# Kernel tuning notes

Measured on AMD Instinct MI355X. Metric: run time of the kernel, lower is better.

## Reference

```python
import math
import jax, jax.numpy as jnp
import numpy as np

NUM_HEADS = 16
HEAD_DIM = 64


def circular_rel_bias(L, slope=1.0):
    idx = jnp.arange(L)
    d = jnp.abs(idx[None, :] - idx[:, None])
    d = jnp.minimum(d, L - d).astype(jnp.float32)
    return -slope * d  # [L, L]


def setup_inputs() -> dict:
    key = jax.random.key(0)
    kq, kk, kv, km = jax.random.split(key, 4)
    B, L, HD = 2, 2048, NUM_HEADS * HEAD_DIM
    return {
        "query_states": jax.random.normal(kq, (B, L, HD), dtype=jnp.float32),
        "key_states": jax.random.normal(kk, (B, L, HD), dtype=jnp.float32),
        "value_states": jax.random.normal(kv, (B, L, HD), dtype=jnp.float32),
        "mask": jax.random.randint(km, (B, L), 0, 2, dtype=jnp.int32),
    }


def reference(query_states, key_states, value_states, mask):
    B, L, _ = query_states.shape
    H, D = NUM_HEADS, HEAD_DIM
    q = query_states.reshape(B, L, H, D).transpose(0, 2, 1, 3)  # [B,H,L,D]
    k = key_states.reshape(B, L, H, D).transpose(0, 2, 1, 3)
    v = value_states.reshape(B, L, H, D).transpose(0, 2, 1, 3)

    scores = jnp.einsum("bhqd,bhkd->bhqk", q, k) / math.sqrt(D)
    scores = scores + circular_rel_bias(L)[None, None, :, :]
    # mask == 0 -> -1e9 on key positions
    scores = jnp.where((mask == 0)[:, None, None, :], jnp.float32(-1e9), scores)
    weights = jax.nn.softmax(scores, axis=-1)
    out = jnp.einsum("bhqk,bhkd->bhqd", weights, v)
    return out.transpose(0, 2, 1, 3).reshape(B, L, H * D)
```

## Files before the change

kernel.cpp:

```cpp
#include <hip/hip_runtime.h>

#define NH 16
#define HD 64
#define LSEQ 2048
#define BQ 128
#define BK 64
#define NQT (LSEQ / BQ)
#define RS (NH * HD)
#define NTILE 4

typedef __bf16 bf16x8 __attribute__((ext_vector_type(8)));
typedef float f32x4 __attribute__((ext_vector_type(4)));

#define EXP_NEG8 0.00033546262790251185f

__global__ __launch_bounds__(512, 4)
void attn_kernel(const float* __restrict__ Q,
                 const float* __restrict__ K,
                 const float* __restrict__ V,
                 const int* __restrict__ Mk,
                 float* __restrict__ Out)
{
    __shared__ alignas(16) char smem_raw[4 * 64 * 72 * 2];
    __shared__ alignas(16) __bf16 sP[8][16][72];
    __bf16* kvb = (__bf16*)smem_raw;

    const int tid  = threadIdx.x;
    const int wave = tid >> 6;
    const int lane = tid & 63;
    const int ln   = lane & 15;
    const int quad = lane >> 4;

    const unsigned bid = blockIdx.x;
    const unsigned w   = (bid & 7u) * 64u + (bid >> 3);
    const int qt = w & (NQT - 1);
    const int bh = w >> 4;
    const int b  = bh >> 4;
    const int h  = bh & 15;

    const int q0   = qt * BQ;
    const int qrow = q0 + wave * 16;

    const size_t bh_off = ((size_t)b * LSEQ) * RS + (size_t)h * HD;
    const float* gQ = Q + bh_off;
    const float* gK = K + bh_off;
    const float* gV = V + bh_off;
    const int*   gM = Mk + (size_t)b * LSEQ;
    float*       gO = Out + bh_off;

    int srow[2], sc4[2];
#pragma unroll
    for (int i = 0; i < 2; ++i) { int idx = tid + i * 512; srow[i] = idx >> 4; sc4[i] = idx & 15; }

    bf16x8 qfrag[2];
#pragma unroll
    for (int c = 0; c < 2; ++c) {
        const float* src = gQ + (size_t)(qrow + ln) * RS + c * 32 + quad * 8;
        float4 f0 = *(const float4*)(src);
        float4 f1 = *(const float4*)(src + 4);
        bf16x8 t;
        t[0] = (__bf16)(f0.x * 0.125f); t[1] = (__bf16)(f0.y * 0.125f);
        t[2] = (__bf16)(f0.z * 0.125f); t[3] = (__bf16)(f0.w * 0.125f);
        t[4] = (__bf16)(f1.x * 0.125f); t[5] = (__bf16)(f1.y * 0.125f);
        t[6] = (__bf16)(f1.z * 0.125f); t[7] = (__bf16)(f1.w * 0.125f);
        qfrag[c] = t;
    }

    f32x4 o_acc[4];
#pragma unroll
    for (int i = 0; i < 4; ++i) o_acc[i] = f32x4{0.f, 0.f, 0.f, 0.f};
    float l_part[4] = {0.f, 0.f, 0.f, 0.f};

    int k0s[NTILE];
#pragma unroll
    for (int j = 0; j < NTILE; ++j) k0s[j] = ((2 * qt + 31 + j) & 31) * BK;

    float4 kreg[2], vreg[2];
    int mr[4];
#pragma unroll
    for (int i = 0; i < 2; ++i) {
        kreg[i] = *(const float4*)(gK + (size_t)(k0s[0] + srow[i]) * RS + sc4[i] * 4);
        vreg[i] = *(const float4*)(gV + (size_t)(k0s[0] + srow[i]) * RS + sc4[i] * 4);
    }
#pragma unroll
    for (int t = 0; t < 4; ++t) mr[t] = gM[k0s[0] + t * 16 + ln];

#pragma unroll
    for (int j = 0; j < NTILE; ++j) {
        const int bb = j & 1;
        __bf16* sKb = kvb + bb * 4608;
        __bf16* sVb = kvb + 9216 + bb * 4608;

#pragma unroll
        for (int i = 0; i < 2; ++i) {
            float4 f = kreg[i];
            __bf16* dst = sKb + srow[i] * 72 + sc4[i] * 4;
            dst[0] = (__bf16)f.x; dst[1] = (__bf16)f.y;
            dst[2] = (__bf16)f.z; dst[3] = (__bf16)f.w;
            float4 g = vreg[i];
            const int vk = srow[i] ^ ((sc4[i] & 7) << 3);
            sVb[(sc4[i] * 4 + 0) * 72 + vk] = (__bf16)g.x;
            sVb[(sc4[i] * 4 + 1) * 72 + vk] = (__bf16)g.y;
            sVb[(sc4[i] * 4 + 2) * 72 + vk] = (__bf16)g.z;
            sVb[(sc4[i] * 4 + 3) * 72 + vk] = (__bf16)g.w;
        }
        float mm[4];
#pragma unroll
        for (int t = 0; t < 4; ++t) mm[t] = mr[t] ? EXP_NEG8 : 0.f;

        if (j + 1 < NTILE) {
            const int k0n = k0s[j + 1];
#pragma unroll
            for (int i = 0; i < 2; ++i) {
                kreg[i] = *(const float4*)(gK + (size_t)(k0n + srow[i]) * RS + sc4[i] * 4);
                vreg[i] = *(const float4*)(gV + (size_t)(k0n + srow[i]) * RS + sc4[i] * 4);
            }
#pragma unroll
            for (int t = 0; t < 4; ++t) mr[t] = gM[k0n + t * 16 + ln];
        }
        __syncthreads();

        const int k0 = k0s[j];
        f32x4 s[4];
#pragma unroll
        for (int t = 0; t < 4; ++t) {
            f32x4 acc = f32x4{0.f, 0.f, 0.f, 0.f};
#pragma unroll
            for (int ch = 0; ch < 2; ++ch) {
                bf16x8 bk = *(const bf16x8*)(sKb + (t * 16 + ln) * 72 + ch * 32 + quad * 8);
                acc = __builtin_amdgcn_mfma_f32_16x16x32_bf16(qfrag[ch], bk, acc, 0, 0, 0);
            }
            s[t] = acc;
        }

        const int qg0 = qrow + quad * 4;
#pragma unroll
        for (int t = 0; t < 4; ++t) {
            const int kg = k0 + t * 16 + ln;
#pragma unroll
            for (int r = 0; r < 4; ++r) {
                int dd = qg0 + r - kg; dd = dd < 0 ? -dd : dd;
                int d2 = LSEQ - dd; dd = d2 < dd ? d2 : dd;
                float p = __expf(s[t][r] - (float)dd) * mm[t];
                l_part[r] += p;
                sP[wave][quad * 4 + r][(t * 16 + ln) ^ (quad << 3)] = (__bf16)p;
            }
        }

#pragma unroll
        for (int ch = 0; ch < 2; ++ch) {
            bf16x8 pa = *(const bf16x8*)&sP[wave][ln][(ch * 32 + quad * 8) ^ ((ln >> 2) << 3)];
#pragma unroll
            for (int nt = 0; nt < 4; ++nt) {
                const int vr = nt * 16 + ln;
                const int vc = (ch * 32 + quad * 8) ^ (((vr >> 2) & 7) << 3);
                bf16x8 bv = *(const bf16x8*)(sVb + vr * 72 + vc);
                o_acc[nt] = __builtin_amdgcn_mfma_f32_16x16x32_bf16(pa, bv, o_acc[nt], 0, 0, 0);
            }
        }
    }

    float inv[4];
#pragma unroll
    for (int r = 0; r < 4; ++r) {
        float l = l_part[r];
#pragma unroll
        for (int off = 1; off < 16; off <<= 1)
            l += __shfl_xor(l, off, 64);
        inv[r] = 1.f / l;
    }

    __syncthreads();
    float* oscr = (float*)smem_raw;
#pragma unroll
    for (int r = 0; r < 4; ++r)
#pragma unroll
        for (int nt = 0; nt < 4; ++nt)
            oscr[(wave * 16 + quad * 4 + r) * 68 + nt * 16 + ln] = o_acc[nt][r] * inv[r];
    __syncthreads();

#pragma unroll
    for (int p = 0; p < 4; ++p) {
        int f   = tid + p * 512;
        int row = f >> 4;
        int c4  = f & 15;
        float4 val = *(const float4*)&oscr[row * 68 + c4 * 4];
        *(float4*)(gO + (size_t)(q0 + row) * RS + c4 * 4) = val;
    }
}

extern "C" void kernel_launch(void* const* d_in, const int* in_sizes, int n_in,
                              void* d_out, int out_size, void* d_ws, size_t ws_size,
                              hipStream_t stream) {
    const float* Q  = (const float*)d_in[0];
    const float* K  = (const float*)d_in[1];
    const float* V  = (const float*)d_in[2];
    const int*   Mk = (const int*)d_in[3];
    float*       O  = (float*)d_out;

    dim3 grid(2 * NH * NQT);
    dim3 block(512);
    attn_kernel<<<grid, block, 0, stream>>>(Q, K, V, Mk, O);
}
```

Before: 107.7 us.

## Keep P in registers via transposed S MFMA and permuted V layout

Computes S transposed by swapping the MFMA operands, so each lane's accumulator elements form the P operand of the PV MFMA directly. This removes the per-wave sP shared-memory round trip and the associated LDS writes and reads. V is stored with a permuted key slot so the register P ordering matches. The key mask is loaded once per tile with a ballot into a 64-bit mask, the row-sum reduction becomes fewer shuffles, and the block-index swizzle is dropped, which may change L2 locality.

```diff
diff --git a/kernel.cpp b/kernel.cpp
--- a/kernel.cpp
+++ b/kernel.cpp
@@ -22,7 +22,6 @@
                  float* __restrict__ Out)
 {
     __shared__ alignas(16) char smem_raw[4 * 64 * 72 * 2];
-    __shared__ alignas(16) __bf16 sP[8][16][72];
     __bf16* kvb = (__bf16*)smem_raw;
 
     const int tid  = threadIdx.x;
@@ -31,10 +30,8 @@
     const int ln   = lane & 15;
     const int quad = lane >> 4;
 
-    const unsigned bid = blockIdx.x;
-    const unsigned w   = (bid & 7u) * 64u + (bid >> 3);
-    const int qt = w & (NQT - 1);
-    const int bh = w >> 4;
+    const int qt = blockIdx.x & (NQT - 1);
+    const int bh = blockIdx.x >> 4;
     const int b  = bh >> 4;
     const int h  = bh & 15;
 
@@ -51,6 +48,13 @@
     int srow[2], sc4[2];
 #pragma unroll
     for (int i = 0; i < 2; ++i) { int idx = tid + i * 512; srow[i] = idx >> 4; sc4[i] = idx & 15; }
+
+    int vslot[2];
+#pragma unroll
+    for (int i = 0; i < 2; ++i) {
+        int k = srow[i];
+        vslot[i] = (k & 32) | ((k & 12) << 1) | ((k & 16) >> 2) | (k & 3);
+    }
 
     bf16x8 qfrag[2];
 #pragma unroll
@@ -69,21 +73,19 @@
     f32x4 o_acc[4];
 #pragma unroll
     for (int i = 0; i < 4; ++i) o_acc[i] = f32x4{0.f, 0.f, 0.f, 0.f};
-    float l_part[4] = {0.f, 0.f, 0.f, 0.f};
+    float l_part = 0.f;
 
     int k0s[NTILE];
 #pragma unroll
     for (int j = 0; j < NTILE; ++j) k0s[j] = ((2 * qt + 31 + j) & 31) * BK;
 
     float4 kreg[2], vreg[2];
-    int mr[4];
 #pragma unroll
     for (int i = 0; i < 2; ++i) {
         kreg[i] = *(const float4*)(gK + (size_t)(k0s[0] + srow[i]) * RS + sc4[i] * 4);
         vreg[i] = *(const float4*)(gV + (size_t)(k0s[0] + srow[i]) * RS + sc4[i] * 4);
     }
-#pragma unroll
-    for (int t = 0; t < 4; ++t) mr[t] = gM[k0s[0] + t * 16 + ln];
+    unsigned long long mbits = __ballot(gM[k0s[0] + lane] != 0);
 
 #pragma unroll
     for (int j = 0; j < NTILE; ++j) {
@@ -98,15 +100,13 @@
             dst[0] = (__bf16)f.x; dst[1] = (__bf16)f.y;
             dst[2] = (__bf16)f.z; dst[3] = (__bf16)f.w;
             float4 g = vreg[i];
-            const int vk = srow[i] ^ ((sc4[i] & 7) << 3);
+            const int vk = vslot[i] ^ ((sc4[i] & 7) << 3);
             sVb[(sc4[i] * 4 + 0) * 72 + vk] = (__bf16)g.x;
             sVb[(sc4[i] * 4 + 1) * 72 + vk] = (__bf16)g.y;
             sVb[(sc4[i] * 4 + 2) * 72 + vk] = (__bf16)g.z;
             sVb[(sc4[i] * 4 + 3) * 72 + vk] = (__bf16)g.w;
         }
-        float mm[4];
-#pragma unroll
-        for (int t = 0; t < 4; ++t) mm[t] = mr[t] ? EXP_NEG8 : 0.f;
+        const unsigned long long mb = mbits;
 
         if (j + 1 < NTILE) {
             const int k0n = k0s[j + 1];
@@ -115,8 +115,7 @@
                 kreg[i] = *(const float4*)(gK + (size_t)(k0n + srow[i]) * RS + sc4[i] * 4);
                 vreg[i] = *(const float4*)(gV + (size_t)(k0n + srow[i]) * RS + sc4[i] * 4);
             }
-#pragma unroll
-            for (int t = 0; t < 4; ++t) mr[t] = gM[k0n + t * 16 + ln];
+            mbits = __ballot(gM[k0n + lane] != 0);
         }
         __syncthreads();
 
@@ -127,29 +126,34 @@
             f32x4 acc = f32x4{0.f, 0.f, 0.f, 0.f};
 #pragma unroll
             for (int ch = 0; ch < 2; ++ch) {
-                bf16x8 bk = *(const bf16x8*)(sKb + (t * 16 + ln) * 72 + ch * 32 + quad * 8);
-                acc = __builtin_amdgcn_mfma_f32_16x16x32_bf16(qfrag[ch], bk, acc, 0, 0, 0);
+                bf16x8 ak = *(const bf16x8*)(sKb + (t * 16 + ln) * 72 + ch * 32 + quad * 8);
+                acc = __builtin_amdgcn_mfma_f32_16x16x32_bf16(ak, qfrag[ch], acc, 0, 0, 0);
             }
             s[t] = acc;
         }
 
-        const int qg0 = qrow + quad * 4;
+        const int qg = qrow + ln;
 #pragma unroll
         for (int t = 0; t < 4; ++t) {
-            const int kg = k0 + t * 16 + ln;
+            const unsigned nib = (unsigned)(mb >> (t * 16 + quad * 4)) & 0xFu;
 #pragma unroll
             for (int r = 0; r < 4; ++r) {
-                int dd = qg0 + r - kg; dd = dd < 0 ? -dd : dd;
+                const int kg = k0 + t * 16 + quad * 4 + r;
+                int dd = qg - kg; dd = dd < 0 ? -dd : dd;
                 int d2 = LSEQ - dd; dd = d2 < dd ? d2 : dd;
-                float p = __expf(s[t][r] - (float)dd) * mm[t];
-                l_part[r] += p;
-                sP[wave][quad * 4 + r][(t * 16 + ln) ^ (quad << 3)] = (__bf16)p;
+                float mmv = ((nib >> r) & 1u) ? EXP_NEG8 : 0.f;
+                float p = __expf(s[t][r] - (float)dd) * mmv;
+                l_part += p;
+                s[t][r] = p;
             }
         }
 
 #pragma unroll
         for (int ch = 0; ch < 2; ++ch) {
-            bf16x8 pa = *(const bf16x8*)&sP[wave][ln][(ch * 32 + quad * 8) ^ ((ln >> 2) << 3)];
+            bf16x8 pa;
+#pragma unroll
+            for (int e = 0; e < 8; ++e)
+                pa[e] = (__bf16)s[ch * 2 + (e >> 2)][e & 3];
 #pragma unroll
             for (int nt = 0; nt < 4; ++nt) {
                 const int vr = nt * 16 + ln;
@@ -160,15 +164,13 @@
         }
     }
 
+    float lf = l_part;
+    lf += __shfl_xor(lf, 16, 64);
+    lf += __shfl_xor(lf, 32, 64);
     float inv[4];
 #pragma unroll
-    for (int r = 0; r < 4; ++r) {
-        float l = l_part[r];
-#pragma unroll
-        for (int off = 1; off < 16; off <<= 1)
-            l += __shfl_xor(l, off, 64);
-        inv[r] = 1.f / l;
-    }
+    for (int r = 0; r < 4; ++r)
+        inv[r] = 1.f / __shfl(lf, quad * 4 + r, 16);
 
     __syncthreads();
     float* oscr = (float*)smem_raw;
```

Result: faster. 103.8 us (-3.6%).
